# Kernel optimization log

Measured on AMD Instinct MI355X. Metric: run time of the kernel, lower is better.

## Reference

```python
import jax, jax.numpy as jnp
import numpy as np

EPS_IN = 1e-5   # torch InstanceNorm2d default eps
EPS_VAR = 1e-6  # clamp floor on attention-weighted variance


def _inorm(x):
    # x: (b, c, t); InstanceNorm2d with affine=False normalizes over spatial dims
    m = x.mean(axis=-1, keepdims=True)
    v = x.var(axis=-1, keepdims=True)  # biased variance, matches torch eval-mode IN
    return (x - m) / jnp.sqrt(v + EPS_IN)


def setup_inputs() -> dict:
    key = jax.random.key(0)
    ks = jax.random.split(key, 9)
    b, t, d = 4, 4096, 256
    sc = 1.0 / np.sqrt(d).astype(np.float32)
    return {
        "fc": jax.random.normal(ks[0], (b, t, d), jnp.float32),
        "fs": jax.random.normal(ks[1], (b, t, d), jnp.float32),
        "fcs": jax.random.normal(ks[2], (b, t, d), jnp.float32),
        "Wf": jax.random.normal(ks[3], (d, d), jnp.float32) * sc,
        "bf": jax.random.normal(ks[4], (d,), jnp.float32) * 0.01,
        "Wg": jax.random.normal(ks[5], (d, d), jnp.float32) * sc,
        "bg": jax.random.normal(ks[6], (d,), jnp.float32) * 0.01,
        "Wh": jax.random.normal(ks[7], (d, d), jnp.float32) * sc,
        "bh": jax.random.normal(ks[8], (d,), jnp.float32) * 0.01,
    }


def reference(fc, fs, fcs, Wf, bf, Wg, bg, Wh, bh):
    # (b, t, d) -> channel-first flat (b, d, t); 1x1 conv == per-token linear
    fc_t = jnp.swapaxes(fc, 1, 2)
    fs_t = jnp.swapaxes(fs, 1, 2)
    fcs_t = jnp.swapaxes(fcs, 1, 2)

    Q = jnp.einsum('oc,bct->bto', Wf, _inorm(fc_t)) + bf                 # (b,t,d)
    K = jnp.einsum('oc,bct->bot', Wg, _inorm(fs_t)) + bg[None, :, None]  # (b,d,t)
    V = jnp.einsum('oc,bct->bto', Wh, fs_t) + bh                         # (b,t,d)

    A = jax.nn.softmax(jnp.einsum('btd,bdu->btu', Q, K), axis=-1)        # (b,t,t)
    M = jnp.einsum('btu,bud->btd', A, V)                                 # mean
    Var = jnp.einsum('btu,bud->btd', A, V * V) - M * M                   # E[v^2]-E[v]^2
    S = jnp.sqrt(jnp.maximum(Var, EPS_VAR))

    out_t = jnp.swapaxes(S, 1, 2) * _inorm(fcs_t) + jnp.swapaxes(M, 1, 2)  # (b,d,t)
    return jnp.swapaxes(out_t, 1, 2)  # (b, t, d)
```

## Files before the change

### kernel.cpp

```cpp
#include <hip/hip_runtime.h>
#include <math.h>

#define B 4
#define T 4096
#define D 256
#define NCH 16
#define CHT (T / NCH)
#define KC 32
#define NCHUNK (T / KC)

typedef __attribute__((ext_vector_type(8))) _Float16 half8;
typedef __attribute__((ext_vector_type(4))) _Float16 half4;
typedef __attribute__((ext_vector_type(4))) float f32x4;

__global__ __launch_bounds__(256) void k_prep(
    const float* __restrict__ fc, const float* __restrict__ fs,
    const float* __restrict__ fcs, float* __restrict__ part,
    const float* __restrict__ Wf, const float* __restrict__ Wg,
    const float* __restrict__ Wh, _Float16* __restrict__ Whi,
    _Float16* __restrict__ Wlo)
{
    int blk = blockIdx.x;
    if (blk < 192) {
        int tensor = blk / (B * NCH);
        int rem = blk % (B * NCH);
        int b = rem / NCH, ch = rem % NCH;
        const float* x = (tensor == 0) ? fc : ((tensor == 1) ? fs : fcs);
        int c = threadIdx.x;
        const float* p = x + ((size_t)b * T + (size_t)ch * CHT) * D + c;
        float s = 0.f, ss = 0.f;
        for (int t = 0; t < CHT; ++t) {
            float v = p[(size_t)t * D];
            s += v; ss += v * v;
        }
        float* o = part + (((size_t)tensor * B + b) * NCH + ch) * 2 * D;
        o[c] = s;
        o[D + c] = ss;
    } else {
        int base = (blk - 192) * 2048;
        #pragma unroll
        for (int i = 0; i < 8; ++i) {
            int idx = base + threadIdx.x + i * 256;
            int which = idx >> 16, rc = idx & 65535;
            const float* Wsrc = (which == 0) ? Wf : ((which == 1) ? Wg : Wh);
            float v = Wsrc[rc];
            _Float16 h = (_Float16)v;
            float l = v - (float)h;
            Whi[idx] = h;
            Wlo[idx] = (_Float16)l;
        }
    }
}

__global__ __launch_bounds__(256) void k_gemm3(
    const float* __restrict__ fc, const float* __restrict__ fs,
    const _Float16* __restrict__ Whi, const _Float16* __restrict__ Wlo,
    const float* __restrict__ bf, const float* __restrict__ bg,
    const float* __restrict__ bh, const float* __restrict__ part,
    _Float16* __restrict__ Qg, _Float16* __restrict__ Kg,
    _Float16* __restrict__ oV, _Float16* __restrict__ oV2h,
    _Float16* __restrict__ oV2l)
{
    __shared__ _Float16 Xl[64 * 256];
    __shared__ float mean_s[256], rstd_s[256];
    const int which = blockIdx.x >> 8;
    const int m0 = (blockIdx.x & 255) * 64;
    const int b = m0 / T;
    const int tid = threadIdx.x;
    const float* x = (which == 0) ? fc : fs;
    const float* bias = (which == 0) ? bf : ((which == 1) ? bg : bh);
    const _Float16* Wh_ = Whi + which * 65536;
    const _Float16* Wl_ = Wlo + which * 65536;
    const int use_norm = (which != 2);

    if (use_norm) {
        int c = tid;
        const float* pp = part + (((size_t)which * B + b) * NCH) * 2 * D;
        float s = 0.f, ss = 0.f;
        for (int ch = 0; ch < NCH; ++ch) {
            s  += pp[(size_t)ch * 2 * D + c];
            ss += pp[(size_t)ch * 2 * D + D + c];
        }
        float mean = s / (float)T;
        float var  = ss / (float)T - mean * mean;
        mean_s[c] = mean;
        rstd_s[c] = rsqrtf(var + 1e-5f);
    }
    __syncthreads();

    #pragma unroll
    for (int j = 0; j < 16; ++j) {
        int idx = tid + j * 256;
        int m = idx >> 6, c4 = idx & 63;
        float4 v = *(const float4*)(x + ((size_t)(m0 + m)) * D + c4 * 4);
        if (use_norm) {
            int c = c4 * 4;
            v.x = (v.x - mean_s[c + 0]) * rstd_s[c + 0];
            v.y = (v.y - mean_s[c + 1]) * rstd_s[c + 1];
            v.z = (v.z - mean_s[c + 2]) * rstd_s[c + 2];
            v.w = (v.w - mean_s[c + 3]) * rstd_s[c + 3];
        }
        half4 h;
        h[0] = (_Float16)v.x; h[1] = (_Float16)v.y;
        h[2] = (_Float16)v.z; h[3] = (_Float16)v.w;
        *(half4*)&Xl[m * 256 + ((c4 * 4) ^ ((m & 7) << 3))] = h;
    }
    __syncthreads();

    const int l = tid & 63, w = tid >> 6;
    const int lo16 = l & 15, hi4 = l >> 4;
    const int row = w * 16 + lo16;

    float bias_v[16];
    #pragma unroll
    for (int nt = 0; nt < 16; ++nt) bias_v[nt] = bias[nt * 16 + lo16];

    f32x4 acc[16];
    #pragma unroll
    for (int nt = 0; nt < 16; ++nt) acc[nt] = (f32x4){0.f, 0.f, 0.f, 0.f};

    #pragma unroll
    for (int kk = 0; kk < 8; ++kk) {
        half8 a = *(const half8*)&Xl[row * 256 + ((kk * 32 + hi4 * 8) ^ ((row & 7) << 3))];
        #pragma unroll
        for (int nt = 0; nt < 16; ++nt) {
            size_t wo = (size_t)(nt * 16 + lo16) * 256 + kk * 32 + hi4 * 8;
            half8 bhf = *(const half8*)(Wh_ + wo);
            acc[nt] = __builtin_amdgcn_mfma_f32_16x16x32_f16(a, bhf, acc[nt], 0, 0, 0);
            half8 blf = *(const half8*)(Wl_ + wo);
            acc[nt] = __builtin_amdgcn_mfma_f32_16x16x32_f16(a, blf, acc[nt], 0, 0, 0);
        }
    }

    if (which != 2) {
        _Float16* out1 = (which == 0) ? Qg : Kg;
        #pragma unroll
        for (int nt = 0; nt < 16; ++nt)
            #pragma unroll
            for (int r = 0; r < 4; ++r) {
                int t = m0 + w * 16 + hi4 * 4 + r;
                out1[(size_t)t * D + nt * 16 + lo16] = (_Float16)(acc[nt][r] + bias_v[nt]);
            }
    } else {
        int t0 = (m0 % T) + w * 16 + hi4 * 4;
        #pragma unroll
        for (int nt = 0; nt < 16; ++nt) {
            int o = nt * 16 + lo16;
            half4 vh, h4, l4;
            #pragma unroll
            for (int r = 0; r < 4; ++r) {
                float v = acc[nt][r] + bias_v[nt];
                _Float16 vhh = (_Float16)v;
                float f2 = (float)vhh * (float)vhh;
                _Float16 hh = (_Float16)f2;
                float fl = f2 - (float)hh;
                vh[r] = vhh; h4[r] = hh; l4[r] = (_Float16)fl;
            }
            size_t base = ((size_t)b * D + o) * T + t0;
            *(half4*)(oV   + base) = vh;
            *(half4*)(oV2h + base) = h4;
            *(half4*)(oV2l + base) = l4;
        }
    }
}

__global__ __launch_bounds__(512, 1) void k_attn(
    const _Float16* __restrict__ Qg, const _Float16* __restrict__ Kg,
    const _Float16* __restrict__ Vtg, const _Float16* __restrict__ V2hg,
    const _Float16* __restrict__ V2lg, const float* __restrict__ fcs,
    const float* __restrict__ part, float* __restrict__ out)
{
    __shared__ __align__(16) _Float16 Kl [2][32 * 256];
    __shared__ __align__(16) _Float16 Vl [2][256 * 32];
    __shared__ __align__(16) _Float16 V2h[2][256 * 32];
    __shared__ __align__(16) _Float16 Pl [2][64 * 32];
    __shared__ float corr_lds[2][64];
    __shared__ float l_lds[64];
    __shared__ int   flags[2][4];
    __shared__ float mfc_s[256], rfc_s[256];

    const int tid = threadIdx.x;
    const int l = tid & 63;
    const int w = tid >> 6;
    const int swz = (blockIdx.x & 7) * 32 + (blockIdx.x >> 3);
    const int b  = swz >> 6;
    const int q0 = (swz & 63) << 6;
    const int lo16 = l & 15, hi4 = l >> 4;

    const _Float16* KgB  = Kg   + (size_t)b * T * D;
    const _Float16* VtB  = Vtg  + (size_t)b * D * T;
    const _Float16* V2hB = V2hg + (size_t)b * D * T;
    const _Float16* V2lB = V2lg + (size_t)b * D * T;

    if (tid < 256) {
        int c = tid;
        const float* pp = part + (((size_t)2 * B + b) * NCH) * 2 * D;
        float s = 0.f, ss = 0.f;
        for (int ch = 0; ch < NCH; ++ch) {
            s  += pp[(size_t)ch * 2 * D + c];
            ss += pp[(size_t)ch * 2 * D + D + c];
        }
        float mean = s / (float)T;
        float var  = ss / (float)T - mean * mean;
        mfc_s[c] = mean;
        rfc_s[c] = rsqrtf(var + 1e-5f);
    }

    half8 qf[8];
    if (w < 4) {
        const _Float16* qp = Qg + ((size_t)(b * T + q0 + 16 * w + lo16)) * D + hi4 * 8;
        #pragma unroll
        for (int kk = 0; kk < 8; ++kk) qf[kk] = *(const half8*)(qp + kk * 32);
    }

    int v2off[2];
    #pragma unroll
    for (int jj = 0; jj < 2; ++jj)
        v2off[jj] = ((2 * w + jj) * 16 + lo16) * T + hi4 * 8;

    f32x4 accM[4][2], accE[4][2];
    #pragma unroll
    for (int qs = 0; qs < 4; ++qs)
        #pragma unroll
        for (int jj = 0; jj < 2; ++jj) {
            accM[qs][jj] = (f32x4){0.f, 0.f, 0.f, 0.f};
            accE[qs][jj] = (f32x4){0.f, 0.f, 0.f, 0.f};
        }
    float m_run[4] = {-1e9f, -1e9f, -1e9f, -1e9f};
    float lv[4] = {0.f, 0.f, 0.f, 0.f};

    const int t2 = tid & 255;
    half8 vr[4], vhr[4];

    auto do_rescale = [&](int pb) {
        #pragma unroll
        for (int qs = 0; qs < 4; ++qs) {
            if (flags[pb][qs]) {
                #pragma unroll
                for (int r = 0; r < 4; ++r) {
                    float c = corr_lds[pb][qs * 16 + hi4 * 4 + r];
                    accM[qs][0][r] *= c; accM[qs][1][r] *= c;
                    accE[qs][0][r] *= c; accE[qs][1][r] *= c;
                }
            }
        }
    };
    auto do_pv = [&](int pb, const half8* b2l) {
        do_rescale(pb);
        half8 pa[4];
        #pragma unroll
        for (int qs = 0; qs < 4; ++qs) {
            int q = qs * 16 + lo16;
            pa[qs] = *(const half8*)&Pl[pb][q * 32 + ((hi4 ^ (q & 3)) << 3)];
        }
        __builtin_amdgcn_s_setprio(1);
        #pragma unroll
        for (int jj = 0; jj < 2; ++jj) {
            int d = (2 * w + jj) * 16 + lo16;
            int p = d * 32 + ((hi4 ^ ((d >> 1) & 3)) << 3);
            half8 bh  = *(const half8*)&Vl[pb][p];
            half8 b2h = *(const half8*)&V2h[pb][p];
            #pragma unroll
            for (int qs = 0; qs < 4; ++qs) {
                accM[qs][jj] = __builtin_amdgcn_mfma_f32_16x16x32_f16(pa[qs], bh,  accM[qs][jj], 0, 0, 0);
                accE[qs][jj] = __builtin_amdgcn_mfma_f32_16x16x32_f16(pa[qs], b2h, accE[qs][jj], 0, 0, 0);
                accE[qs][jj] = __builtin_amdgcn_mfma_f32_16x16x32_f16(pa[qs], b2l[jj], accE[qs][jj], 0, 0, 0);
            }
        }
        __builtin_amdgcn_s_setprio(0);
    };

    if (w >= 4) {
        half8 kr0[4];
        #pragma unroll
        for (int i = 0; i < 4; ++i) {
            int g = t2 + i * 256;
            kr0[i] = *(const half8*)(KgB + (size_t)(g >> 5) * D + (g & 31) * 8);
        }
        #pragma unroll
        for (int i = 0; i < 4; ++i) {
            int g = t2 + i * 256; int d = g >> 2, kg = g & 3;
            size_t off = (size_t)d * T + kg * 8;
            vr[i]  = *(const half8*)(VtB  + off);
            vhr[i] = *(const half8*)(V2hB + off);
        }
        #pragma unroll
        for (int i = 0; i < 4; ++i) {
            int g = t2 + i * 256; int rr = g >> 5, cg = g & 31;
            *(half8*)&Kl[0][rr * 256 + ((cg ^ (rr & 7)) << 3)] = kr0[i];
        }
    }
    __syncthreads();

    for (int kc = 0; kc < NCHUNK; ++kc) {
        const int cb = kc & 1, pb = cb ^ 1;

        half8 b2l[2];
        if (kc > 0) {
            const _Float16* v2b = V2lB + (kc - 1) * KC;
            b2l[0] = *(const half8*)(v2b + v2off[0]);
            b2l[1] = *(const half8*)(v2b + v2off[1]);
        }

        if (w < 4) {
            f32x4 c0 = (f32x4){0.f, 0.f, 0.f, 0.f}, c1 = (f32x4){0.f, 0.f, 0.f, 0.f};

            if (kc == 0) {
                __builtin_amdgcn_s_setprio(1);
                #pragma unroll
                for (int kk = 0; kk < 8; ++kk) {
                    int cg = kk * 4 + hi4;
                    half8 kb0 = *(const half8*)&Kl[cb][lo16 * 256 + ((cg ^ (lo16 & 7)) << 3)];
                    half8 kb1 = *(const half8*)&Kl[cb][(16 + lo16) * 256 + ((cg ^ ((16 + lo16) & 7)) << 3)];
                    c0 = __builtin_amdgcn_mfma_f32_16x16x32_f16(qf[kk], kb0, c0, 0, 0, 0);
                    c1 = __builtin_amdgcn_mfma_f32_16x16x32_f16(qf[kk], kb1, c1, 0, 0, 0);
                }
                __builtin_amdgcn_s_setprio(0);
            } else {
                do_rescale(pb);
                half8 pa[4];
                #pragma unroll
                for (int qs = 0; qs < 4; ++qs) {
                    int q = qs * 16 + lo16;
                    pa[qs] = *(const half8*)&Pl[pb][q * 32 + ((hi4 ^ (q & 3)) << 3)];
                }
                half8 bhv[2], b2h[2];
                #pragma unroll
                for (int jj = 0; jj < 2; ++jj) {
                    int d = (2 * w + jj) * 16 + lo16;
                    int p = d * 32 + ((hi4 ^ ((d >> 1) & 3)) << 3);
                    bhv[jj] = *(const half8*)&Vl[pb][p];
                    b2h[jj] = *(const half8*)&V2h[pb][p];
                }
                __builtin_amdgcn_s_setprio(1);
                #pragma unroll
                for (int kk = 0; kk < 8; ++kk) {
                    int cg = kk * 4 + hi4;
                    half8 kb0 = *(const half8*)&Kl[cb][lo16 * 256 + ((cg ^ (lo16 & 7)) << 3)];
                    half8 kb1 = *(const half8*)&Kl[cb][(16 + lo16) * 256 + ((cg ^ ((16 + lo16) & 7)) << 3)];
                    c0 = __builtin_amdgcn_mfma_f32_16x16x32_f16(qf[kk], kb0, c0, 0, 0, 0);
                    c1 = __builtin_amdgcn_mfma_f32_16x16x32_f16(qf[kk], kb1, c1, 0, 0, 0);
                    #pragma unroll
                    for (int i = 0; i < 3; ++i) {
                        int t = kk * 3 + i;
                        if (t < 8) {
                            int qs = t & 3, jj = t >> 2;
                            accM[qs][jj] = __builtin_amdgcn_mfma_f32_16x16x32_f16(pa[qs], bhv[jj], accM[qs][jj], 0, 0, 0);
                        } else if (t < 16) {
                            int k = t - 8; int qs = k & 3, jj = k >> 2;
                            accE[qs][jj] = __builtin_amdgcn_mfma_f32_16x16x32_f16(pa[qs], b2h[jj], accE[qs][jj], 0, 0, 0);
                        } else {
                            int k = t - 16; int qs = k & 3, jj = k >> 2;
                            accE[qs][jj] = __builtin_amdgcn_mfma_f32_16x16x32_f16(pa[qs], b2l[jj], accE[qs][jj], 0, 0, 0);
                        }
                    }
                }
                __builtin_amdgcn_s_setprio(0);
            }

            float cm[4];
            #pragma unroll
            for (int r = 0; r < 4; ++r) cm[r] = fmaxf(c0[r], c1[r]);
            float tmax = fmaxf(fmaxf(cm[0] - m_run[0], cm[1] - m_run[1]),
                               fmaxf(cm[2] - m_run[2], cm[3] - m_run[3]));
            int flagv = 0;
            if (__any(tmax > 10.f)) {
                flagv = 1;
                float corr[4];
                #pragma unroll
                for (int r = 0; r < 4; ++r) {
                    float rm = cm[r];
                    rm = fmaxf(rm, __shfl_xor(rm, 1));
                    rm = fmaxf(rm, __shfl_xor(rm, 2));
                    rm = fmaxf(rm, __shfl_xor(rm, 4));
                    rm = fmaxf(rm, __shfl_xor(rm, 8));
                    float mn = fmaxf(m_run[r], rm);
                    corr[r] = __expf(m_run[r] - mn);
                    m_run[r] = mn;
                    lv[r] *= corr[r];
                }
                if (lo16 == 0) {
                    #pragma unroll
                    for (int r = 0; r < 4; ++r)
                        corr_lds[cb][w * 16 + hi4 * 4 + r] = corr[r];
                }
            }
            if (l == 0) flags[cb][w] = flagv;

            float p0[4], p1[4];
            #pragma unroll
            for (int r = 0; r < 4; ++r) {
                p0[r] = __expf(c0[r] - m_run[r]);
                p1[r] = __expf(c1[r] - m_run[r]);
                lv[r] += p0[r] + p1[r];
            }
            #pragma unroll
            for (int r = 0; r < 4; ++r) {
                int q = 16 * w + hi4 * 4 + r;
                int ka = lo16, kb = 16 + lo16;
                Pl[cb][q * 32 + (((ka >> 3) ^ (q & 3)) << 3) + (ka & 7)] = (_Float16)p0[r];
                Pl[cb][q * 32 + (((kb >> 3) ^ (q & 3)) << 3) + (kb & 7)] = (_Float16)p1[r];
            }
        } else {
            #pragma unroll
            for (int i = 0; i < 4; ++i) {
                int g = t2 + i * 256; int d = g >> 2, kg = g & 3;
                int p = d * 32 + ((kg ^ ((d >> 1) & 3)) << 3);
                *(half8*)&Vl[cb][p]  = vr[i];
                *(half8*)&V2h[cb][p] = vhr[i];
            }

            half8 kr[4];
            const bool doK = (kc + 1 < NCHUNK);
            if (doK) {
                int kn = (kc + 1) * KC;
                #pragma unroll
                for (int i = 0; i < 4; ++i) {
                    int g = t2 + i * 256;
                    kr[i] = *(const half8*)(KgB + (size_t)(kn + (g >> 5)) * D + (g & 31) * 8);
                }
                #pragma unroll
                for (int i = 0; i < 4; ++i) {
                    int g = t2 + i * 256; int d = g >> 2, kg = g & 3;
                    size_t off = (size_t)d * T + kn + kg * 8;
                    vr[i]  = *(const half8*)(VtB  + off);
                    vhr[i] = *(const half8*)(V2hB + off);
                }
            }

            if (kc > 0) do_pv(pb, b2l);

            if (doK) {
                #pragma unroll
                for (int i = 0; i < 4; ++i) {
                    int g = t2 + i * 256; int rr = g >> 5, cg = g & 31;
                    *(half8*)&Kl[cb ^ 1][rr * 256 + ((cg ^ (rr & 7)) << 3)] = kr[i];
                }
            }
        }
        __syncthreads();
    }

    {
        half8 b2l[2];
        const _Float16* v2b = V2lB + (NCHUNK - 1) * KC;
        b2l[0] = *(const half8*)(v2b + v2off[0]);
        b2l[1] = *(const half8*)(v2b + v2off[1]);
        do_pv((NCHUNK - 1) & 1, b2l);
    }

    if (w < 4) {
        #pragma unroll
        for (int r = 0; r < 4; ++r) {
            float lr = lv[r];
            lr += __shfl_xor(lr, 1);
            lr += __shfl_xor(lr, 2);
            lr += __shfl_xor(lr, 4);
            lr += __shfl_xor(lr, 8);
            if (lo16 == 0) l_lds[w * 16 + hi4 * 4 + r] = lr;
        }
    }
    __syncthreads();

    #pragma unroll
    for (int qs = 0; qs < 4; ++qs) {
        #pragma unroll
        for (int r = 0; r < 4; ++r) {
            float linv = 1.f / l_lds[qs * 16 + hi4 * 4 + r];
            int q = q0 + qs * 16 + hi4 * 4 + r;
            size_t rowb = ((size_t)(b * T + q)) * D;
            #pragma unroll
            for (int jj = 0; jj < 2; ++jj) {
                int d = (2 * w + jj) * 16 + lo16;
                float M  = accM[qs][jj][r] * linv;
                float E2 = accE[qs][jj][r] * linv;
                float S  = sqrtf(fmaxf(E2 - M * M, 1e-6f));
                float f  = fcs[rowb + d];
                out[rowb + d] = S * ((f - mfc_s[d]) * rfc_s[d]) + M;
            }
        }
    }
}

extern "C" void kernel_launch(void* const* d_in, const int* in_sizes, int n_in,
                              void* d_out, int out_size, void* d_ws, size_t ws_size,
                              hipStream_t stream)
{
    const float* fc  = (const float*)d_in[0];
    const float* fs  = (const float*)d_in[1];
    const float* fcs = (const float*)d_in[2];
    const float* Wf  = (const float*)d_in[3];
    const float* bf  = (const float*)d_in[4];
    const float* Wg  = (const float*)d_in[5];
    const float* bg  = (const float*)d_in[6];
    const float* Wh  = (const float*)d_in[7];
    const float* bh  = (const float*)d_in[8];
    float* out = (float*)d_out;

    char* ws = (char*)d_ws;
    float* part  = (float*)(ws + (64 << 10));
    _Float16* Whi = (_Float16*)(ws + (512 << 10));
    _Float16* Wlo = Whi + 3 * 65536;
    _Float16* Qg   = (_Float16*)(ws + (2 << 20));
    _Float16* Kg   = Qg  + (size_t)B * T * D;
    _Float16* Vtg  = Kg  + (size_t)B * T * D;
    _Float16* V2hg = Vtg + (size_t)B * T * D;
    _Float16* V2lg = V2hg + (size_t)B * T * D;

    k_prep<<<288, 256, 0, stream>>>(fc, fs, fcs, part, Wf, Wg, Wh, Whi, Wlo);

    k_gemm3<<<3 * 256, 256, 0, stream>>>(fc, fs, Whi, Wlo, bf, bg, bh, part,
                                         Qg, Kg, Vtg, V2hg, V2lg);

    k_attn<<<B * (T / 64), 512, 0, stream>>>(Qg, Kg, Vtg, V2hg, V2lg, fcs, part, out);
}
```

Measured before the change: 298.6 us.

## Shrink attention tile to 32 queries, 256-thread blocks, two per CU

```diff
diff --git a/kernel.cpp b/kernel.cpp
--- a/kernel.cpp
+++ b/kernel.cpp
@@ -164,7 +164,7 @@
     }
 }
 
-__global__ __launch_bounds__(512, 1) void k_attn(
+__global__ __launch_bounds__(256, 2) void k_attn(
     const _Float16* __restrict__ Qg, const _Float16* __restrict__ Kg,
     const _Float16* __restrict__ Vtg, const _Float16* __restrict__ V2hg,
     const _Float16* __restrict__ V2lg, const float* __restrict__ fcs,
@@ -172,19 +172,18 @@
 {
     __shared__ __align__(16) _Float16 Kl [2][32 * 256];
     __shared__ __align__(16) _Float16 Vl [2][256 * 32];
-    __shared__ __align__(16) _Float16 V2h[2][256 * 32];
-    __shared__ __align__(16) _Float16 Pl [2][64 * 32];
-    __shared__ float corr_lds[2][64];
-    __shared__ float l_lds[64];
-    __shared__ int   flags[2][4];
+    __shared__ __align__(16) _Float16 Pl [2][32 * 32];
+    __shared__ float corr_lds[2][32];
+    __shared__ float l_lds[32];
+    __shared__ int   flags[2][2];
     __shared__ float mfc_s[256], rfc_s[256];
 
     const int tid = threadIdx.x;
     const int l = tid & 63;
     const int w = tid >> 6;
-    const int swz = (blockIdx.x & 7) * 32 + (blockIdx.x >> 3);
-    const int b  = swz >> 6;
-    const int q0 = (swz & 63) << 6;
+    const int swz = (blockIdx.x & 7) * 64 + (blockIdx.x >> 3);
+    const int b  = swz >> 7;
+    const int q0 = (swz & 127) << 5;
     const int lo16 = l & 15, hi4 = l >> 4;
 
     const _Float16* KgB  = Kg   + (size_t)b * T * D;
@@ -207,86 +206,83 @@
     }
 
     half8 qf[8];
-    if (w < 4) {
+    if (w < 2) {
         const _Float16* qp = Qg + ((size_t)(b * T + q0 + 16 * w + lo16)) * D + hi4 * 8;
         #pragma unroll
         for (int kk = 0; kk < 8; ++kk) qf[kk] = *(const half8*)(qp + kk * 32);
     }
 
-    int v2off[2];
-    #pragma unroll
-    for (int jj = 0; jj < 2; ++jj)
-        v2off[jj] = ((2 * w + jj) * 16 + lo16) * T + hi4 * 8;
-
-    f32x4 accM[4][2], accE[4][2];
-    #pragma unroll
-    for (int qs = 0; qs < 4; ++qs)
-        #pragma unroll
-        for (int jj = 0; jj < 2; ++jj) {
+    int voff[4];
+    #pragma unroll
+    for (int jj = 0; jj < 4; ++jj)
+        voff[jj] = ((4 * w + jj) * 16 + lo16) * T + hi4 * 8;
+
+    f32x4 accM[2][4], accE[2][4];
+    #pragma unroll
+    for (int qs = 0; qs < 2; ++qs)
+        #pragma unroll
+        for (int jj = 0; jj < 4; ++jj) {
             accM[qs][jj] = (f32x4){0.f, 0.f, 0.f, 0.f};
             accE[qs][jj] = (f32x4){0.f, 0.f, 0.f, 0.f};
         }
     float m_run[4] = {-1e9f, -1e9f, -1e9f, -1e9f};
     float lv[4] = {0.f, 0.f, 0.f, 0.f};
 
-    const int t2 = tid & 255;
-    half8 vr[4], vhr[4];
+    const int t2 = tid & 127;
+    half8 vr[8];
 
     auto do_rescale = [&](int pb) {
         #pragma unroll
-        for (int qs = 0; qs < 4; ++qs) {
+        for (int qs = 0; qs < 2; ++qs) {
             if (flags[pb][qs]) {
                 #pragma unroll
                 for (int r = 0; r < 4; ++r) {
                     float c = corr_lds[pb][qs * 16 + hi4 * 4 + r];
-                    accM[qs][0][r] *= c; accM[qs][1][r] *= c;
-                    accE[qs][0][r] *= c; accE[qs][1][r] *= c;
+                    #pragma unroll
+                    for (int jj = 0; jj < 4; ++jj) { accM[qs][jj][r] *= c; accE[qs][jj][r] *= c; }
                 }
             }
         }
     };
-    auto do_pv = [&](int pb, const half8* b2l) {
+    auto do_pv = [&](int pb, const half8* b2h, const half8* b2l) {
         do_rescale(pb);
-        half8 pa[4];
-        #pragma unroll
-        for (int qs = 0; qs < 4; ++qs) {
+        half8 pa[2];
+        #pragma unroll
+        for (int qs = 0; qs < 2; ++qs) {
             int q = qs * 16 + lo16;
             pa[qs] = *(const half8*)&Pl[pb][q * 32 + ((hi4 ^ (q & 3)) << 3)];
         }
         __builtin_amdgcn_s_setprio(1);
         #pragma unroll
-        for (int jj = 0; jj < 2; ++jj) {
-            int d = (2 * w + jj) * 16 + lo16;
+        for (int jj = 0; jj < 4; ++jj) {
+            int d = (4 * w + jj) * 16 + lo16;
             int p = d * 32 + ((hi4 ^ ((d >> 1) & 3)) << 3);
-            half8 bh  = *(const half8*)&Vl[pb][p];
-            half8 b2h = *(const half8*)&V2h[pb][p];
-            #pragma unroll
-            for (int qs = 0; qs < 4; ++qs) {
-                accM[qs][jj] = __builtin_amdgcn_mfma_f32_16x16x32_f16(pa[qs], bh,  accM[qs][jj], 0, 0, 0);
-                accE[qs][jj] = __builtin_amdgcn_mfma_f32_16x16x32_f16(pa[qs], b2h, accE[qs][jj], 0, 0, 0);
+            half8 bh = *(const half8*)&Vl[pb][p];
+            #pragma unroll
+            for (int qs = 0; qs < 2; ++qs) {
+                accM[qs][jj] = __builtin_amdgcn_mfma_f32_16x16x32_f16(pa[qs], bh, accM[qs][jj], 0, 0, 0);
+                accE[qs][jj] = __builtin_amdgcn_mfma_f32_16x16x32_f16(pa[qs], b2h[jj], accE[qs][jj], 0, 0, 0);
                 accE[qs][jj] = __builtin_amdgcn_mfma_f32_16x16x32_f16(pa[qs], b2l[jj], accE[qs][jj], 0, 0, 0);
             }
         }
         __builtin_amdgcn_s_setprio(0);
     };
 
-    if (w >= 4) {
-        half8 kr0[4];
-        #pragma unroll
-        for (int i = 0; i < 4; ++i) {
-            int g = t2 + i * 256;
+    if (w >= 2) {
+        half8 kr0[8];
+        #pragma unroll
+        for (int i = 0; i < 8; ++i) {
+            int g = t2 + i * 128;
             kr0[i] = *(const half8*)(KgB + (size_t)(g >> 5) * D + (g & 31) * 8);
         }
         #pragma unroll
-        for (int i = 0; i < 4; ++i) {
-            int g = t2 + i * 256; int d = g >> 2, kg = g & 3;
-            size_t off = (size_t)d * T + kg * 8;
-            vr[i]  = *(const half8*)(VtB  + off);
-            vhr[i] = *(const half8*)(V2hB + off);
-        }
-        #pragma unroll
-        for (int i = 0; i < 4; ++i) {
-            int g = t2 + i * 256; int rr = g >> 5, cg = g & 31;
+        for (int i = 0; i < 8; ++i) {
+            int g = t2 + i * 128; int d = g >> 2, kg = g & 3;
+            vr[i] = *(const half8*)(VtB + (size_t)d * T + kg * 8);
+        }
+        #pragma unroll
+        for (int i = 0; i < 8; ++i) {
+            int g = t2 + i * 128; int rr = g >> 5, cg = g & 31;
             *(half8*)&Kl[0][rr * 256 + ((cg ^ (rr & 7)) << 3)] = kr0[i];
         }
     }
@@ -295,14 +291,17 @@
     for (int kc = 0; kc < NCHUNK; ++kc) {
         const int cb = kc & 1, pb = cb ^ 1;
 
-        half8 b2l[2];
+        half8 b2h[4], b2l[4];
         if (kc > 0) {
-            const _Float16* v2b = V2lB + (kc - 1) * KC;
-            b2l[0] = *(const half8*)(v2b + v2off[0]);
-            b2l[1] = *(const half8*)(v2b + v2off[1]);
-        }
-
-        if (w < 4) {
+            int kp = (kc - 1) * KC;
+            #pragma unroll
+            for (int jj = 0; jj < 4; ++jj) {
+                b2h[jj] = *(const half8*)(V2hB + kp + voff[jj]);
+                b2l[jj] = *(const half8*)(V2lB + kp + voff[jj]);
+            }
+        }
+
+        if (w < 2) {
             f32x4 c0 = (f32x4){0.f, 0.f, 0.f, 0.f}, c1 = (f32x4){0.f, 0.f, 0.f, 0.f};
 
             if (kc == 0) {
@@ -318,19 +317,18 @@
                 __builtin_amdgcn_s_setprio(0);
             } else {
                 do_rescale(pb);
-                half8 pa[4];
-                #pragma unroll
-                for (int qs = 0; qs < 4; ++qs) {
+                half8 pa[2];
+                #pragma unroll
+                for (int qs = 0; qs < 2; ++qs) {
                     int q = qs * 16 + lo16;
                     pa[qs] = *(const half8*)&Pl[pb][q * 32 + ((hi4 ^ (q & 3)) << 3)];
                 }
-                half8 bhv[2], b2h[2];
-                #pragma unroll
-                for (int jj = 0; jj < 2; ++jj) {
-                    int d = (2 * w + jj) * 16 + lo16;
+                half8 bhv[4];
+                #pragma unroll
+                for (int jj = 0; jj < 4; ++jj) {
+                    int d = (4 * w + jj) * 16 + lo16;
                     int p = d * 32 + ((hi4 ^ ((d >> 1) & 3)) << 3);
                     bhv[jj] = *(const half8*)&Vl[pb][p];
-                    b2h[jj] = *(const half8*)&V2h[pb][p];
                 }
                 __builtin_amdgcn_s_setprio(1);
                 #pragma unroll
@@ -344,13 +342,13 @@
                     for (int i = 0; i < 3; ++i) {
                         int t = kk * 3 + i;
                         if (t < 8) {
-                            int qs = t & 3, jj = t >> 2;
+                            int qs = t & 1, jj = (t >> 1) & 3;
                             accM[qs][jj] = __builtin_amdgcn_mfma_f32_16x16x32_f16(pa[qs], bhv[jj], accM[qs][jj], 0, 0, 0);
                         } else if (t < 16) {
-                            int k = t - 8; int qs = k & 3, jj = k >> 2;
+                            int k = t - 8; int qs = k & 1, jj = (k >> 1) & 3;
                             accE[qs][jj] = __builtin_amdgcn_mfma_f32_16x16x32_f16(pa[qs], b2h[jj], accE[qs][jj], 0, 0, 0);
                         } else {
-                            int k = t - 16; int qs = k & 3, jj = k >> 2;
+                            int k = t - 16; int qs = k & 1, jj = (k >> 1) & 3;
                             accE[qs][jj] = __builtin_amdgcn_mfma_f32_16x16x32_f16(pa[qs], b2l[jj], accE[qs][jj], 0, 0, 0);
                         }
                     }
@@ -403,37 +401,34 @@
             }
         } else {
             #pragma unroll
-            for (int i = 0; i < 4; ++i) {
-                int g = t2 + i * 256; int d = g >> 2, kg = g & 3;
+            for (int i = 0; i < 8; ++i) {
+                int g = t2 + i * 128; int d = g >> 2, kg = g & 3;
                 int p = d * 32 + ((kg ^ ((d >> 1) & 3)) << 3);
-                *(half8*)&Vl[cb][p]  = vr[i];
-                *(half8*)&V2h[cb][p] = vhr[i];
-            }
-
-            half8 kr[4];
+                *(half8*)&Vl[cb][p] = vr[i];
+            }
+
+            half8 kr[8];
             const bool doK = (kc + 1 < NCHUNK);
             if (doK) {
                 int kn = (kc + 1) * KC;
                 #pragma unroll
-                for (int i = 0; i < 4; ++i) {
-                    int g = t2 + i * 256;
+                for (int i = 0; i < 8; ++i) {
+                    int g = t2 + i * 128;
                     kr[i] = *(const half8*)(KgB + (size_t)(kn + (g >> 5)) * D + (g & 31) * 8);
                 }
                 #pragma unroll
-                for (int i = 0; i < 4; ++i) {
-                    int g = t2 + i * 256; int d = g >> 2, kg = g & 3;
-                    size_t off = (size_t)d * T + kn + kg * 8;
-                    vr[i]  = *(const half8*)(VtB  + off);
-                    vhr[i] = *(const half8*)(V2hB + off);
-                }
-            }
-
-            if (kc > 0) do_pv(pb, b2l);
+                for (int i = 0; i < 8; ++i) {
+                    int g = t2 + i * 128; int d = g >> 2, kg = g & 3;
+                    vr[i] = *(const half8*)(VtB + (size_t)d * T + kn + kg * 8);
+                }
+            }
+
+            if (kc > 0) do_pv(pb, b2h, b2l);
 
             if (doK) {
                 #pragma unroll
-                for (int i = 0; i < 4; ++i) {
-                    int g = t2 + i * 256; int rr = g >> 5, cg = g & 31;
+                for (int i = 0; i < 8; ++i) {
+                    int g = t2 + i * 128; int rr = g >> 5, cg = g & 31;
                     *(half8*)&Kl[cb ^ 1][rr * 256 + ((cg ^ (rr & 7)) << 3)] = kr[i];
                 }
             }
@@ -442,14 +437,17 @@
     }
 
     {
-        half8 b2l[2];
-        const _Float16* v2b = V2lB + (NCHUNK - 1) * KC;
-        b2l[0] = *(const half8*)(v2b + v2off[0]);
-        b2l[1] = *(const half8*)(v2b + v2off[1]);
-        do_pv((NCHUNK - 1) & 1, b2l);
-    }
-
-    if (w < 4) {
+        half8 b2h[4], b2l[4];
+        int kp = (NCHUNK - 1) * KC;
+        #pragma unroll
+        for (int jj = 0; jj < 4; ++jj) {
+            b2h[jj] = *(const half8*)(V2hB + kp + voff[jj]);
+            b2l[jj] = *(const half8*)(V2lB + kp + voff[jj]);
+        }
+        do_pv((NCHUNK - 1) & 1, b2h, b2l);
+    }
+
+    if (w < 2) {
         #pragma unroll
         for (int r = 0; r < 4; ++r) {
             float lr = lv[r];
@@ -463,15 +461,15 @@
     __syncthreads();
 
     #pragma unroll
-    for (int qs = 0; qs < 4; ++qs) {
+    for (int qs = 0; qs < 2; ++qs) {
         #pragma unroll
         for (int r = 0; r < 4; ++r) {
             float linv = 1.f / l_lds[qs * 16 + hi4 * 4 + r];
             int q = q0 + qs * 16 + hi4 * 4 + r;
             size_t rowb = ((size_t)(b * T + q)) * D;
             #pragma unroll
-            for (int jj = 0; jj < 2; ++jj) {
-                int d = (2 * w + jj) * 16 + lo16;
+            for (int jj = 0; jj < 4; ++jj) {
+                int d = (4 * w + jj) * 16 + lo16;
                 float M  = accM[qs][jj][r] * linv;
                 float E2 = accE[qs][jj][r] * linv;
                 float S  = sqrtf(fmaxf(E2 - M * M, 1e-6f));
@@ -512,5 +510,5 @@
     k_gemm3<<<3 * 256, 256, 0, stream>>>(fc, fs, Whi, Wlo, bf, bg, bh, part,
                                          Qg, Kg, Vtg, V2hg, V2lg);
 
-    k_attn<<<B * (T / 64), 512, 0, stream>>>(Qg, Kg, Vtg, V2hg, V2lg, fcs, part, out);
+    k_attn<<<B * (T / 32), 256, 0, stream>>>(Qg, Kg, Vtg, V2hg, V2lg, fcs, part, out);
 }
```

New measurement: 669.1 us. +124.0%, slower.
